# Performance work log

Measured on AMD Instinct MI355X. Metric: run time of the kernel, lower is better.

## Reference

```python
import jax, jax.numpy as jnp
import numpy as np

N_NODES = 100000
N_EDGES = 1600000
D_IN = 128
HID = 128
N_CLS = 10
N_GRAPHS = 128


def _gcn_conv(x, W, b, src, dst, dis, n):
    # x' = W x; out[i] = sum_{(j->i)} d_j^{-1/2} d_i^{-1/2} x'_j ; then + bias
    h = x @ W  # [N, out]
    norm = dis[src] * dis[dst]  # [E_tot]
    msg = h[src] * norm[:, None]  # gather + scale (irregular access)
    out = jax.ops.segment_sum(msg, dst, num_segments=n)  # scatter-add
    return out + b


def setup_inputs() -> dict:
    key = jax.random.key(0)
    ks = jax.random.split(key, 12)
    x = jax.random.normal(ks[0], (N_NODES, D_IN), dtype=jnp.float32)
    edge_index = jax.random.randint(ks[1], (2, N_EDGES), 0, N_NODES, dtype=jnp.int64)
    batch = jnp.sort(jax.random.randint(ks[2], (N_NODES,), 0, N_GRAPHS, dtype=jnp.int64))
    drop_u = jax.random.uniform(ks[3], (N_NODES, D_IN), dtype=jnp.float32)
    s = lambda k, sh, fan: jax.random.normal(k, sh, dtype=jnp.float32) / np.sqrt(fan)
    return {
        "x": x, "edge_index": edge_index, "batch": batch, "num_graphs": N_GRAPHS,
        "drop_u": drop_u,
        "lin1_w": s(ks[4], (D_IN, D_IN), D_IN), "lin1_b": jnp.zeros((D_IN,), jnp.float32),
        "conv1_w": s(ks[5], (D_IN, HID), D_IN), "conv1_b": jnp.zeros((HID,), jnp.float32),
        "conv2_w": s(ks[6], (HID, HID // 2), HID), "conv2_b": jnp.zeros((HID // 2,), jnp.float32),
        "lin2_w": s(ks[7], (HID // 2, N_CLS), HID // 2), "lin2_b": jnp.zeros((N_CLS,), jnp.float32),
    }


def reference(x, edge_index, batch, num_graphs, drop_u,
              lin1_w, lin1_b, conv1_w, conv1_b, conv2_w, conv2_b, lin2_w, lin2_b):
    n = x.shape[0]
    # add self loops (PyG GCNConv default)
    loop = jnp.arange(n, dtype=edge_index.dtype)
    src = jnp.concatenate([edge_index[0], loop])
    dst = jnp.concatenate([edge_index[1], loop])
    deg = jax.ops.segment_sum(jnp.ones_like(dst, dtype=x.dtype), dst, num_segments=n)
    dis = jnp.where(deg > 0, jax.lax.rsqrt(deg), 0.0)  # deg^{-1/2}

    h = x @ lin1_w + lin1_b
    h = _gcn_conv(h, conv1_w, conv1_b, src, dst, dis, n)
    # dropout p=0.5 (training mode in original): keep where u >= 0.5, scale by 2
    h = h * (drop_u >= 0.5).astype(h.dtype) * 2.0
    h = jax.nn.relu(h)
    h = _gcn_conv(h, conv2_w, conv2_b, src, dst, dis, n)
    # global mean pool over graph ids
    sums = jax.ops.segment_sum(h, batch, num_segments=num_graphs)
    cnts = jax.ops.segment_sum(jnp.ones((n,), h.dtype), batch, num_segments=num_graphs)
    pooled = sums / jnp.maximum(cnts, 1.0)[:, None]
    return pooled @ lin2_w + lin2_b
```

## Files before the change

### kernel.cpp

```cpp
#include <hip/hip_runtime.h>
#include <hip/hip_bf16.h>

#define DIN   128
#define HID2  64
#define NCLS  10
#define NGRAPH 128
#define SCAN_CHUNK 1024
#define NBLK 256
#define NBKT_MAX 512
#define CAP 6144

typedef __attribute__((ext_vector_type(8))) short bf16x8;
typedef __attribute__((ext_vector_type(4))) float f32x4;

__device__ __forceinline__ void atomAddF(float* p, float v) {
    unsafeAtomicAdd(p, v);
}

__device__ __forceinline__ unsigned short f2bf(float f) {
    unsigned int u = __float_as_uint(f);
    u += 0x7fffu + ((u >> 16) & 1u);
    return (unsigned short)(u >> 16);
}

__global__ __launch_bounds__(128) void k_w12(const float* __restrict__ lw,
                                             const float* __restrict__ lb,
                                             const float* __restrict__ cw,
                                             float* __restrict__ W12,
                                             float* __restrict__ c1preb) {
    int i = blockIdx.x, j = threadIdx.x;
    const float* arow = (i < 128) ? (lw + i * 128) : lb;
    float acc = 0.f;
#pragma unroll 8
    for (int k = 0; k < 128; ++k) acc += arow[k] * cw[k * 128 + j];
    if (i < 128) W12[i * 128 + j] = acc;
    else         c1preb[j] = acc;
}

__global__ __launch_bounds__(256) void k_zero(float* p, int n) {
    int i = blockIdx.x * 256 + threadIdx.x;
    if (i < n) p[i] = 0.0f;
}

__global__ __launch_bounds__(256) void k_bhist(const int* __restrict__ dst,
                                               int* __restrict__ bh, int E, int nbkt) {
    __shared__ int lh[NBKT_MAX];
    for (int i = threadIdx.x; i < nbkt; i += 256) lh[i] = 0;
    __syncthreads();
    for (int e = blockIdx.x * 256 + threadIdx.x; e < E; e += NBLK * 256)
        atomicAdd(&lh[__builtin_nontemporal_load(dst + e) >> 8], 1);
    __syncthreads();
    for (int i = threadIdx.x; i < nbkt; i += 256) bh[i * NBLK + blockIdx.x] = lh[i];
}

__global__ __launch_bounds__(256) void k_scan_part(const int* __restrict__ cnt,
                                                   int* __restrict__ part, int n) {
    int base = blockIdx.x * SCAN_CHUNK + threadIdx.x * 4;
    int s = 0;
#pragma unroll
    for (int j = 0; j < 4; ++j) { int i = base + j; if (i < n) s += cnt[i]; }
#pragma unroll
    for (int o = 32; o > 0; o >>= 1) s += __shfl_down(s, o);
    __shared__ int wsum[4];
    if ((threadIdx.x & 63) == 0) wsum[threadIdx.x >> 6] = s;
    __syncthreads();
    if (threadIdx.x == 0) part[blockIdx.x] = wsum[0] + wsum[1] + wsum[2] + wsum[3];
}
__global__ __launch_bounds__(256) void k_scan_mid(int* __restrict__ part,
                                                  int* __restrict__ total_out,
                                                  int B, int n) {
    __shared__ int sh[256];
    int t = threadIdx.x;
    int v = (t < B) ? part[t] : 0;
    sh[t] = v;
    __syncthreads();
    for (int off = 1; off < 256; off <<= 1) {
        int u = (t >= off) ? sh[t - off] : 0;
        __syncthreads();
        sh[t] += u;
        __syncthreads();
    }
    if (t < B) part[t] = sh[t] - v;
    if (t == 255) total_out[n] = sh[255];
}
__global__ __launch_bounds__(256) void k_scan_fin2(const int* cnt,
                                                   const int* __restrict__ part,
                                                   int* out, int n) {
    __shared__ int sh[256];
    int t = threadIdx.x;
    int base = blockIdx.x * SCAN_CHUNK + t * 4;
    int c[4]; int s = 0;
#pragma unroll
    for (int j = 0; j < 4; ++j) { int i = base + j; c[j] = (i < n) ? cnt[i] : 0; s += c[j]; }
    sh[t] = s;
    __syncthreads();
    for (int off = 1; off < 256; off <<= 1) {
        int u = (t >= off) ? sh[t - off] : 0;
        __syncthreads();
        sh[t] += u;
        __syncthreads();
    }
    int excl = part[blockIdx.x] + sh[t] - s;
#pragma unroll
    for (int j = 0; j < 4; ++j) {
        int i = base + j;
        if (i < n) out[i] = excl;
        excl += c[j];
    }
}

__global__ __launch_bounds__(256) void k_partition(const int* __restrict__ src,
                                                   const int* __restrict__ dst,
                                                   const int* __restrict__ bh,
                                                   int2* __restrict__ pairs, int E, int nbkt) {
    __shared__ int cur[NBKT_MAX];
    for (int i = threadIdx.x; i < nbkt; i += 256) cur[i] = bh[i * NBLK + blockIdx.x];
    __syncthreads();
    for (int e = blockIdx.x * 256 + threadIdx.x; e < E; e += NBLK * 256) {
        int d = __builtin_nontemporal_load(dst + e);
        int s = __builtin_nontemporal_load(src + e);
        int pos = atomicAdd(&cur[d >> 8], 1);
        pairs[pos] = make_int2(d, s);
    }
}

__global__ __launch_bounds__(256) void k_csr_local(const int2* __restrict__ pairs,
                                                   const int* __restrict__ bh,
                                                   int* __restrict__ row_start,
                                                   float* __restrict__ dis,
                                                   int* __restrict__ col,
                                                   int N) {
    __shared__ int cntL[256], scanL[256], curL[256];
    __shared__ int srcbuf[CAP];
    const int tid = threadIdx.x;
    const int lo = blockIdx.x << 8;
    const int bstart = bh[blockIdx.x * NBLK];
    const int bend = bh[(blockIdx.x + 1) * NBLK];
    const int nE = bend - bstart;

    cntL[tid] = 0;
    __syncthreads();
    for (int e = bstart + tid; e < bend; e += 256)
        atomicAdd(&cntL[pairs[e].x & 255], 1);
    __syncthreads();
    const int deg = cntL[tid];
    scanL[tid] = deg;
    __syncthreads();
    for (int off = 1; off < 256; off <<= 1) {
        int u = (tid >= off) ? scanL[tid - off] : 0;
        __syncthreads();
        scanL[tid] += u;
        __syncthreads();
    }
    const int excl = scanL[tid] - deg;
    curL[tid] = excl;
    const int node = lo + tid;
    if (node < N) {
        row_start[node] = bstart + excl;
        dis[node] = rsqrtf((float)(deg + 1));
    } else if (node == N) {
        row_start[N] = bend;
    }
    __syncthreads();
    if (nE <= CAP) {
        for (int e = bstart + tid; e < bend; e += 256) {
            int2 p = pairs[e];
            int pos = atomicAdd(&curL[p.x & 255], 1);
            srcbuf[pos] = p.y;
        }
        __syncthreads();
        for (int i = tid; i < nE; i += 256)
            col[bstart + i] = srcbuf[i];
    } else {
        for (int e = bstart + tid; e < bend; e += 256) {
            int2 p = pairs[e];
            int pos = atomicAdd(&curL[p.x & 255], 1);
            col[bstart + pos] = p.y;
        }
    }
}

template <int NCOL, bool MASK>
__global__ __launch_bounds__(256) void k_gemm_mfma(const float* __restrict__ A,
                                                   const float* __restrict__ W,
                                                   const float* __restrict__ bias,
                                                   const float* __restrict__ du,
                                                   unsigned short* __restrict__ out, int M) {
    constexpr int KP = 136;
    __shared__ unsigned short As[64 * KP];
    __shared__ unsigned short Wt[NCOL * KP];

    const int tid = threadIdx.x;
    const int row0 = blockIdx.x * 64;

    for (int f = tid; f < 2048; f += 256) {
        int r = f >> 5, c4 = f & 31;
        int gr = row0 + r;
        float4 v = make_float4(0.f, 0.f, 0.f, 0.f);
        if (gr < M) {
            v = *(const float4*)(A + (size_t)gr * 128 + c4 * 4);
            if (MASK) {
                float4 u = *(const float4*)(du + (size_t)gr * 128 + c4 * 4);
                v.x = (u.x >= 0.5f) ? 2.f * fmaxf(v.x, 0.f) : 0.f;
                v.y = (u.y >= 0.5f) ? 2.f * fmaxf(v.y, 0.f) : 0.f;
                v.z = (u.z >= 0.5f) ? 2.f * fmaxf(v.z, 0.f) : 0.f;
                v.w = (u.w >= 0.5f) ? 2.f * fmaxf(v.w, 0.f) : 0.f;
            }
        }
        ushort4 b;
        b.x = f2bf(v.x); b.y = f2bf(v.y); b.z = f2bf(v.z); b.w = f2bf(v.w);
        *(ushort4*)(&As[r * KP + c4 * 4]) = b;
    }
    for (int f = tid; f < 32 * NCOL; f += 256) {
        int k = f / (NCOL / 4), n4 = f % (NCOL / 4);
        float4 v = *(const float4*)(W + (size_t)k * NCOL + n4 * 4);
        Wt[(n4 * 4 + 0) * KP + k] = f2bf(v.x);
        Wt[(n4 * 4 + 1) * KP + k] = f2bf(v.y);
        Wt[(n4 * 4 + 2) * KP + k] = f2bf(v.z);
        Wt[(n4 * 4 + 3) * KP + k] = f2bf(v.w);
    }
    __syncthreads();

    const int wave = tid >> 6, lane = tid & 63;
    const int quad = lane >> 4, l16 = lane & 15;
    constexpr int CT = (NCOL == 128) ? 2 : 1;
    const int col0 = wave * 16 * CT;

    f32x4 acc[4][CT];
#pragma unroll
    for (int rt = 0; rt < 4; ++rt)
#pragma unroll
        for (int ct = 0; ct < CT; ++ct) acc[rt][ct] = 0.f;

#pragma unroll
    for (int ks = 0; ks < 4; ++ks) {
        const int kbase = ks * 32 + quad * 8;
        bf16x8 bfr[CT];
#pragma unroll
        for (int ct = 0; ct < CT; ++ct)
            bfr[ct] = *(const bf16x8*)(&Wt[(col0 + ct * 16 + l16) * KP + kbase]);
#pragma unroll
        for (int rt = 0; rt < 4; ++rt) {
            bf16x8 afr = *(const bf16x8*)(&As[(rt * 16 + l16) * KP + kbase]);
#pragma unroll
            for (int ct = 0; ct < CT; ++ct)
                acc[rt][ct] = __builtin_amdgcn_mfma_f32_16x16x32_bf16(afr, bfr[ct], acc[rt][ct], 0, 0, 0);
        }
    }

#pragma unroll
    for (int rt = 0; rt < 4; ++rt)
#pragma unroll
        for (int ct = 0; ct < CT; ++ct) {
            const int c = col0 + ct * 16 + l16;
            const float bv = bias ? bias[c] : 0.f;
#pragma unroll
            for (int reg = 0; reg < 4; ++reg) {
                const int gr = row0 + rt * 16 + quad * 4 + reg;
                if (gr < M) out[(size_t)gr * NCOL + c] = f2bf(acc[rt][ct][reg] + bv);
            }
        }
}

__device__ __forceinline__ void bfacc(uint4 v, float d, float* acc) {
    acc[0] = fmaf(d, __uint_as_float(v.x << 16),        acc[0]);
    acc[1] = fmaf(d, __uint_as_float(v.x & 0xffff0000u), acc[1]);
    acc[2] = fmaf(d, __uint_as_float(v.y << 16),        acc[2]);
    acc[3] = fmaf(d, __uint_as_float(v.y & 0xffff0000u), acc[3]);
    acc[4] = fmaf(d, __uint_as_float(v.z << 16),        acc[4]);
    acc[5] = fmaf(d, __uint_as_float(v.z & 0xffff0000u), acc[5]);
    acc[6] = fmaf(d, __uint_as_float(v.w << 16),        acc[6]);
    acc[7] = fmaf(d, __uint_as_float(v.w & 0xffff0000u), acc[7]);
}

template <int NCOL>
__global__ __launch_bounds__(256) void k_gather(const unsigned short* __restrict__ h,
                                                const int* __restrict__ row_start,
                                                const int* __restrict__ col,
                                                const float* __restrict__ dis,
                                                const float* __restrict__ bias,
                                                float* __restrict__ out, int n) {
    constexpr int LPN = NCOL / 8;
    const int node = (blockIdx.x * 256 + threadIdx.x) / LPN;
    const int l = threadIdx.x % LPN;
    if (node >= n) return;
    const int coff = l * 8;

    const float dn = dis[node];
    float acc[8];
    {
        uint4 v = *(const uint4*)(h + (size_t)node * NCOL + coff);
#pragma unroll
        for (int q = 0; q < 8; ++q) acc[q] = 0.f;
        bfacc(v, dn, acc);
    }

    const int beg = row_start[node], end = row_start[node + 1];
    int j = beg;
    for (; j + 1 < end; j += 2) {
        const int s0 = col[j], s1 = col[j + 1];
        const float d0 = dis[s0], d1 = dis[s1];
        const uint4 v0 = *(const uint4*)(h + (size_t)s0 * NCOL + coff);
        const uint4 v1 = *(const uint4*)(h + (size_t)s1 * NCOL + coff);
        bfacc(v0, d0, acc);
        bfacc(v1, d1, acc);
    }
    if (j < end) {
        const int s0 = col[j];
        const float d0 = dis[s0];
        const uint4 v0 = *(const uint4*)(h + (size_t)s0 * NCOL + coff);
        bfacc(v0, d0, acc);
    }

    float4 r0, r1;
    const float4 b0 = *(const float4*)(bias + coff);
    const float4 b1 = *(const float4*)(bias + coff + 4);
    r0.x = fmaf(dn, acc[0], b0.x); r0.y = fmaf(dn, acc[1], b0.y);
    r0.z = fmaf(dn, acc[2], b0.z); r0.w = fmaf(dn, acc[3], b0.w);
    r1.x = fmaf(dn, acc[4], b1.x); r1.y = fmaf(dn, acc[5], b1.y);
    r1.z = fmaf(dn, acc[6], b1.z); r1.w = fmaf(dn, acc[7], b1.w);
    float* o = out + (size_t)node * NCOL + coff;
    *(float4*)(o) = r0;
    *(float4*)(o + 4) = r1;
}

__global__ __launch_bounds__(256) void k_pool(const float* __restrict__ h,
                                              const int* __restrict__ batch,
                                              float* __restrict__ sums,
                                              float* __restrict__ cnt,
                                              int n) {
    int gid = (blockIdx.x * 256 + threadIdx.x) / 64;
    int f = threadIdx.x % 64;
    int ngroups = gridDim.x * 4;
    int per = (n + ngroups - 1) / ngroups;
    int start = gid * per;
    int end = min(n, start + per);
    if (start >= end) return;
    int cg = batch[start];
    float acc = 0.f;
    int count = 0;
    for (int i = start; i < end; ++i) {
        int b = batch[i];
        if (b != cg) {
            atomAddF(&sums[cg * 64 + f], acc);
            if (f == 0) atomAddF(&cnt[cg], (float)count);
            acc = 0.f; count = 0; cg = b;
        }
        acc += h[(size_t)i * 64 + f];
        ++count;
    }
    atomAddF(&sums[cg * 64 + f], acc);
    if (f == 0) atomAddF(&cnt[cg], (float)count);
}

__global__ __launch_bounds__(64) void k_final(const float* __restrict__ sums,
                                              const float* __restrict__ cnt,
                                              const float* __restrict__ w,
                                              const float* __restrict__ b,
                                              float* __restrict__ out) {
    int g = blockIdx.x, f = threadIdx.x;
    float c = fmaxf(cnt[g], 1.0f);
    float p = sums[g * 64 + f] / c;
#pragma unroll
    for (int cls = 0; cls < NCLS; ++cls) {
        float v = p * w[f * 10 + cls];
#pragma unroll
        for (int o = 32; o > 0; o >>= 1) v += __shfl_down(v, o);
        if (f == 0) out[g * 10 + cls] = v + b[cls];
    }
}

extern "C" void kernel_launch(void* const* d_in, const int* in_sizes, int n_in,
                              void* d_out, int out_size, void* d_ws, size_t ws_size,
                              hipStream_t stream) {
    const float* x       = (const float*)d_in[0];
    const int*   ei      = (const int*)d_in[1];
    const int*   batch   = (const int*)d_in[2];
    const float* drop_u  = (const float*)d_in[4];
    const float* lin1_w  = (const float*)d_in[5];
    const float* lin1_b  = (const float*)d_in[6];
    const float* conv1_w = (const float*)d_in[7];
    const float* conv1_b = (const float*)d_in[8];
    const float* conv2_w = (const float*)d_in[9];
    const float* conv2_b = (const float*)d_in[10];
    const float* lin2_w  = (const float*)d_in[11];
    const float* lin2_b  = (const float*)d_in[12];
    float* out = (float*)d_out;

    const int N = in_sizes[0] / DIN;
    const int E = in_sizes[1] / 2;
    const int* src = ei;
    const int* dst = ei + E;

    const int nbkt = (N + 255) >> 8;
    const int M = nbkt * NBLK;

    float* ws    = (float*)d_ws;
    float* out1  = ws;
    unsigned short* h1b = (unsigned short*)(ws + (size_t)N * 128);
    float* dis   = ws + (size_t)N * 128 + (size_t)N * 64;
    float* W12   = dis + N;
    float* c1pb  = W12 + 16384;
    float* sums  = c1pb + 128;
    float* cntp  = sums + NGRAPH * 64;
    int*   row_start = (int*)(cntp + NGRAPH);
    int*   part  = row_start + N + 2;
    int*   bh    = part + 256;
    int*   col   = bh + NBKT_MAX * NBLK + 2;
    int2*  pairs = (int2*)(col + E);
    unsigned short* h2b = h1b;
    float* out2  = out1;

    k_w12<<<129, 128, 0, stream>>>(lin1_w, lin1_b, conv1_w, W12, c1pb);

    k_bhist<<<NBLK, 256, 0, stream>>>(dst, bh, E, nbkt);
    const int scanB = (M + SCAN_CHUNK - 1) / SCAN_CHUNK;
    k_scan_part<<<scanB, 256, 0, stream>>>(bh, part, M);
    k_scan_mid<<<1, 256, 0, stream>>>(part, bh, scanB, M);
    k_scan_fin2<<<scanB, 256, 0, stream>>>(bh, part, bh, M);
    k_partition<<<NBLK, 256, 0, stream>>>(src, dst, bh, pairs, E, nbkt);
    k_csr_local<<<nbkt, 256, 0, stream>>>(pairs, bh, row_start, dis, col, N);

    const int gemmGrid = (N + 63) / 64;
    k_gemm_mfma<128, false><<<gemmGrid, 256, 0, stream>>>(x, W12, c1pb, nullptr, h1b, N);

    k_gather<128><<<((size_t)N * 16 + 255) / 256, 256, 0, stream>>>(h1b, row_start, col, dis, conv1_b, out1, N);

    k_gemm_mfma<64, true><<<gemmGrid, 256, 0, stream>>>(out1, conv2_w, nullptr, drop_u, h2b, N);

    k_gather<64><<<((size_t)N * 8 + 255) / 256, 256, 0, stream>>>(h2b, row_start, col, dis, conv2_b, out2, N);

    k_zero<<<(NGRAPH * 64 + NGRAPH + 255) / 256, 256, 0, stream>>>(sums, NGRAPH * 64 + NGRAPH);
    k_pool<<<2048, 256, 0, stream>>>(out2, batch, sums, cntp, N);
    k_final<<<NGRAPH, 64, 0, stream>>>(sums, cntp, lin2_w, lin2_b, out);
}
```

Baseline: 410.8 us.

## Pack edge pairs, bf16 intermediates, fuse pooling into second gather, drop zero kernel

Several changes at once. Edge pairs are packed into one 32-bit word (src<<8 | dst&255), which halves partition traffic. The first aggregation now writes bf16 instead of fp32, and a new GEMM reads bf16 with dropout/relu applied on load. The second gather fuses the global mean pool with wave-level reductions and atomics. The zeroing kernel moves into the histogram kernel, and the gather loops unroll by 4. Together these aim to cut memory traffic and launches, at the cost of extra bf16 rounding of the intermediate and a src-index range limit of 24 bits.

```diff
diff --git a/kernel.cpp b/kernel.cpp
--- a/kernel.cpp
+++ b/kernel.cpp
@@ -37,14 +37,12 @@
     else         c1preb[j] = acc;
 }
 
-__global__ __launch_bounds__(256) void k_zero(float* p, int n) {
-    int i = blockIdx.x * 256 + threadIdx.x;
-    if (i < n) p[i] = 0.0f;
-}
-
 __global__ __launch_bounds__(256) void k_bhist(const int* __restrict__ dst,
-                                               int* __restrict__ bh, int E, int nbkt) {
+                                               int* __restrict__ bh, int E, int nbkt,
+                                               float* __restrict__ zbuf, int zn) {
     __shared__ int lh[NBKT_MAX];
+    if (blockIdx.x == 0)
+        for (int i = threadIdx.x; i < zn; i += 256) zbuf[i] = 0.f;
     for (int i = threadIdx.x; i < nbkt; i += 256) lh[i] = 0;
     __syncthreads();
     for (int e = blockIdx.x * 256 + threadIdx.x; e < E; e += NBLK * 256)
@@ -112,7 +110,7 @@
 __global__ __launch_bounds__(256) void k_partition(const int* __restrict__ src,
                                                    const int* __restrict__ dst,
                                                    const int* __restrict__ bh,
-                                                   int2* __restrict__ pairs, int E, int nbkt) {
+                                                   int* __restrict__ pairs, int E, int nbkt) {
     __shared__ int cur[NBKT_MAX];
     for (int i = threadIdx.x; i < nbkt; i += 256) cur[i] = bh[i * NBLK + blockIdx.x];
     __syncthreads();
@@ -120,11 +118,11 @@
         int d = __builtin_nontemporal_load(dst + e);
         int s = __builtin_nontemporal_load(src + e);
         int pos = atomicAdd(&cur[d >> 8], 1);
-        pairs[pos] = make_int2(d, s);
-    }
-}
-
-__global__ __launch_bounds__(256) void k_csr_local(const int2* __restrict__ pairs,
+        pairs[pos] = (s << 8) | (d & 255);
+    }
+}
+
+__global__ __launch_bounds__(256) void k_csr_local(const int* __restrict__ pairs,
                                                    const int* __restrict__ bh,
                                                    int* __restrict__ row_start,
                                                    float* __restrict__ dis,
@@ -141,7 +139,7 @@
     cntL[tid] = 0;
     __syncthreads();
     for (int e = bstart + tid; e < bend; e += 256)
-        atomicAdd(&cntL[pairs[e].x & 255], 1);
+        atomicAdd(&cntL[pairs[e] & 255], 1);
     __syncthreads();
     const int deg = cntL[tid];
     scanL[tid] = deg;
@@ -164,27 +162,26 @@
     __syncthreads();
     if (nE <= CAP) {
         for (int e = bstart + tid; e < bend; e += 256) {
-            int2 p = pairs[e];
-            int pos = atomicAdd(&curL[p.x & 255], 1);
-            srcbuf[pos] = p.y;
+            int p = pairs[e];
+            int pos = atomicAdd(&curL[p & 255], 1);
+            srcbuf[pos] = ((unsigned int)p) >> 8;
         }
         __syncthreads();
         for (int i = tid; i < nE; i += 256)
             col[bstart + i] = srcbuf[i];
     } else {
         for (int e = bstart + tid; e < bend; e += 256) {
-            int2 p = pairs[e];
-            int pos = atomicAdd(&curL[p.x & 255], 1);
-            col[bstart + pos] = p.y;
-        }
-    }
-}
-
-template <int NCOL, bool MASK>
+            int p = pairs[e];
+            int pos = atomicAdd(&curL[p & 255], 1);
+            col[bstart + pos] = ((unsigned int)p) >> 8;
+        }
+    }
+}
+
+template <int NCOL>
 __global__ __launch_bounds__(256) void k_gemm_mfma(const float* __restrict__ A,
                                                    const float* __restrict__ W,
                                                    const float* __restrict__ bias,
-                                                   const float* __restrict__ du,
                                                    unsigned short* __restrict__ out, int M) {
     constexpr int KP = 136;
     __shared__ unsigned short As[64 * KP];
@@ -197,16 +194,7 @@
         int r = f >> 5, c4 = f & 31;
         int gr = row0 + r;
         float4 v = make_float4(0.f, 0.f, 0.f, 0.f);
-        if (gr < M) {
-            v = *(const float4*)(A + (size_t)gr * 128 + c4 * 4);
-            if (MASK) {
-                float4 u = *(const float4*)(du + (size_t)gr * 128 + c4 * 4);
-                v.x = (u.x >= 0.5f) ? 2.f * fmaxf(v.x, 0.f) : 0.f;
-                v.y = (u.y >= 0.5f) ? 2.f * fmaxf(v.y, 0.f) : 0.f;
-                v.z = (u.z >= 0.5f) ? 2.f * fmaxf(v.z, 0.f) : 0.f;
-                v.w = (u.w >= 0.5f) ? 2.f * fmaxf(v.w, 0.f) : 0.f;
-            }
-        }
+        if (gr < M) v = *(const float4*)(A + (size_t)gr * 128 + c4 * 4);
         ushort4 b;
         b.x = f2bf(v.x); b.y = f2bf(v.y); b.z = f2bf(v.z); b.w = f2bf(v.w);
         *(ushort4*)(&As[r * KP + c4 * 4]) = b;
@@ -260,6 +248,80 @@
                 if (gr < M) out[(size_t)gr * NCOL + c] = f2bf(acc[rt][ct][reg] + bv);
             }
         }
+}
+
+__device__ __forceinline__ unsigned int maskbf2(unsigned int w, float ua, float ub) {
+    float a = __uint_as_float(w << 16);
+    float b = __uint_as_float(w & 0xffff0000u);
+    a = (ua >= 0.5f) ? 2.f * fmaxf(a, 0.f) : 0.f;
+    b = (ub >= 0.5f) ? 2.f * fmaxf(b, 0.f) : 0.f;
+    return (unsigned int)f2bf(a) | ((unsigned int)f2bf(b) << 16);
+}
+
+__global__ __launch_bounds__(256) void k_gemm_bf16in(const unsigned short* __restrict__ A,
+                                                     const float* __restrict__ W,
+                                                     const float* __restrict__ du,
+                                                     unsigned short* __restrict__ out, int M) {
+    constexpr int NCOL = 64, KP = 136;
+    __shared__ unsigned short As[64 * KP];
+    __shared__ unsigned short Wt[NCOL * KP];
+
+    const int tid = threadIdx.x;
+    const int row0 = blockIdx.x * 64;
+
+    for (int f = tid; f < 1024; f += 256) {
+        int r = f >> 4, c8 = f & 15;
+        int gr = row0 + r;
+        uint4 b = make_uint4(0u, 0u, 0u, 0u);
+        if (gr < M) {
+            const uint4 v = *(const uint4*)(A + (size_t)gr * 128 + c8 * 8);
+            const float4 u0 = *(const float4*)(du + (size_t)gr * 128 + c8 * 8);
+            const float4 u1 = *(const float4*)(du + (size_t)gr * 128 + c8 * 8 + 4);
+            b.x = maskbf2(v.x, u0.x, u0.y);
+            b.y = maskbf2(v.y, u0.z, u0.w);
+            b.z = maskbf2(v.z, u1.x, u1.y);
+            b.w = maskbf2(v.w, u1.z, u1.w);
+        }
+        *(uint4*)(&As[r * KP + c8 * 8]) = b;
+    }
+    for (int f = tid; f < 32 * NCOL; f += 256) {
+        int k = f / (NCOL / 4), n4 = f % (NCOL / 4);
+        float4 v = *(const float4*)(W + (size_t)k * NCOL + n4 * 4);
+        Wt[(n4 * 4 + 0) * KP + k] = f2bf(v.x);
+        Wt[(n4 * 4 + 1) * KP + k] = f2bf(v.y);
+        Wt[(n4 * 4 + 2) * KP + k] = f2bf(v.z);
+        Wt[(n4 * 4 + 3) * KP + k] = f2bf(v.w);
+    }
+    __syncthreads();
+
+    const int wave = tid >> 6, lane = tid & 63;
+    const int quad = lane >> 4, l16 = lane & 15;
+    const int col0 = wave * 16;
+
+    f32x4 acc[4];
+#pragma unroll
+    for (int rt = 0; rt < 4; ++rt) acc[rt] = 0.f;
+
+#pragma unroll
+    for (int ks = 0; ks < 4; ++ks) {
+        const int kbase = ks * 32 + quad * 8;
+        bf16x8 bfr = *(const bf16x8*)(&Wt[(col0 + l16) * KP + kbase]);
+#pragma unroll
+        for (int rt = 0; rt < 4; ++rt) {
+            bf16x8 afr = *(const bf16x8*)(&As[(rt * 16 + l16) * KP + kbase]);
+            acc[rt] = __builtin_amdgcn_mfma_f32_16x16x32_bf16(afr, bfr, acc[rt], 0, 0, 0);
+        }
+    }
+
+#pragma unroll
+    for (int rt = 0; rt < 4; ++rt) {
+        const int c = col0 + l16;
+#pragma unroll
+        for (int reg = 0; reg < 4; ++reg) {
+            const int gr = row0 + rt * 16 + quad * 4 + reg;
+            if (gr < M) out[(size_t)gr * NCOL + c] = f2bf(acc[rt][reg]);
+        }
+    }
 }
 
 __device__ __forceinline__ void bfacc(uint4 v, float d, float* acc) {
@@ -273,23 +335,21 @@
     acc[7] = fmaf(d, __uint_as_float(v.w & 0xffff0000u), acc[7]);
 }
 
-template <int NCOL>
-__global__ __launch_bounds__(256) void k_gather(const unsigned short* __restrict__ h,
-                                                const int* __restrict__ row_start,
-                                                const int* __restrict__ col,
-                                                const float* __restrict__ dis,
-                                                const float* __restrict__ bias,
-                                                float* __restrict__ out, int n) {
-    constexpr int LPN = NCOL / 8;
-    const int node = (blockIdx.x * 256 + threadIdx.x) / LPN;
-    const int l = threadIdx.x % LPN;
+__global__ __launch_bounds__(256) void k_gather_h1(const unsigned short* __restrict__ h,
+                                                   const int* __restrict__ row_start,
+                                                   const int* __restrict__ col,
+                                                   const float* __restrict__ dis,
+                                                   const float* __restrict__ bias,
+                                                   unsigned short* __restrict__ outb, int n) {
+    const int node = (blockIdx.x * 256 + (int)threadIdx.x) >> 4;
+    const int l = threadIdx.x & 15;
     if (node >= n) return;
     const int coff = l * 8;
 
     const float dn = dis[node];
     float acc[8];
     {
-        uint4 v = *(const uint4*)(h + (size_t)node * NCOL + coff);
+        uint4 v = *(const uint4*)(h + (size_t)node * 128 + coff);
 #pragma unroll
         for (int q = 0; q < 8; ++q) acc[q] = 0.f;
         bfacc(v, dn, acc);
@@ -297,60 +357,115 @@
 
     const int beg = row_start[node], end = row_start[node + 1];
     int j = beg;
-    for (; j + 1 < end; j += 2) {
-        const int s0 = col[j], s1 = col[j + 1];
-        const float d0 = dis[s0], d1 = dis[s1];
-        const uint4 v0 = *(const uint4*)(h + (size_t)s0 * NCOL + coff);
-        const uint4 v1 = *(const uint4*)(h + (size_t)s1 * NCOL + coff);
+    for (; j + 3 < end; j += 4) {
+        const int s0 = col[j], s1 = col[j + 1], s2 = col[j + 2], s3 = col[j + 3];
+        const float d0 = dis[s0], d1 = dis[s1], d2 = dis[s2], d3 = dis[s3];
+        const uint4 v0 = *(const uint4*)(h + (size_t)s0 * 128 + coff);
+        const uint4 v1 = *(const uint4*)(h + (size_t)s1 * 128 + coff);
+        const uint4 v2 = *(const uint4*)(h + (size_t)s2 * 128 + coff);
+        const uint4 v3 = *(const uint4*)(h + (size_t)s3 * 128 + coff);
         bfacc(v0, d0, acc);
         bfacc(v1, d1, acc);
-    }
-    if (j < end) {
+        bfacc(v2, d2, acc);
+        bfacc(v3, d3, acc);
+    }
+    for (; j < end; ++j) {
         const int s0 = col[j];
         const float d0 = dis[s0];
-        const uint4 v0 = *(const uint4*)(h + (size_t)s0 * NCOL + coff);
+        const uint4 v0 = *(const uint4*)(h + (size_t)s0 * 128 + coff);
         bfacc(v0, d0, acc);
     }
 
-    float4 r0, r1;
     const float4 b0 = *(const float4*)(bias + coff);
     const float4 b1 = *(const float4*)(bias + coff + 4);
-    r0.x = fmaf(dn, acc[0], b0.x); r0.y = fmaf(dn, acc[1], b0.y);
-    r0.z = fmaf(dn, acc[2], b0.z); r0.w = fmaf(dn, acc[3], b0.w);
-    r1.x = fmaf(dn, acc[4], b1.x); r1.y = fmaf(dn, acc[5], b1.y);
-    r1.z = fmaf(dn, acc[6], b1.z); r1.w = fmaf(dn, acc[7], b1.w);
-    float* o = out + (size_t)node * NCOL + coff;
-    *(float4*)(o) = r0;
-    *(float4*)(o + 4) = r1;
-}
-
-__global__ __launch_bounds__(256) void k_pool(const float* __restrict__ h,
-                                              const int* __restrict__ batch,
-                                              float* __restrict__ sums,
-                                              float* __restrict__ cnt,
-                                              int n) {
-    int gid = (blockIdx.x * 256 + threadIdx.x) / 64;
-    int f = threadIdx.x % 64;
-    int ngroups = gridDim.x * 4;
-    int per = (n + ngroups - 1) / ngroups;
-    int start = gid * per;
-    int end = min(n, start + per);
-    if (start >= end) return;
-    int cg = batch[start];
-    float acc = 0.f;
-    int count = 0;
-    for (int i = start; i < end; ++i) {
-        int b = batch[i];
-        if (b != cg) {
-            atomAddF(&sums[cg * 64 + f], acc);
-            if (f == 0) atomAddF(&cnt[cg], (float)count);
-            acc = 0.f; count = 0; cg = b;
-        }
-        acc += h[(size_t)i * 64 + f];
-        ++count;
-    }
-    atomAddF(&sums[cg * 64 + f], acc);
-    if (f == 0) atomAddF(&cnt[cg], (float)count);
+    const float r0 = fmaf(dn, acc[0], b0.x), r1 = fmaf(dn, acc[1], b0.y);
+    const float r2 = fmaf(dn, acc[2], b0.z), r3 = fmaf(dn, acc[3], b0.w);
+    const float r4 = fmaf(dn, acc[4], b1.x), r5 = fmaf(dn, acc[5], b1.y);
+    const float r6 = fmaf(dn, acc[6], b1.z), r7 = fmaf(dn, acc[7], b1.w);
+    uint4 o;
+    o.x = (unsigned int)f2bf(r0) | ((unsigned int)f2bf(r1) << 16);
+    o.y = (unsigned int)f2bf(r2) | ((unsigned int)f2bf(r3) << 16);
+    o.z = (unsigned int)f2bf(r4) | ((unsigned int)f2bf(r5) << 16);
+    o.w = (unsigned int)f2bf(r6) | ((unsigned int)f2bf(r7) << 16);
+    *(uint4*)(outb + (size_t)node * 128 + coff) = o;
+}
+
+__global__ __launch_bounds__(256) void k_gather_pool(const unsigned short* __restrict__ h,
+                                                     const int* __restrict__ row_start,
+                                                     const int* __restrict__ col,
+                                                     const float* __restrict__ dis,
+                                                     const float* __restrict__ bias,
+                                                     const int* __restrict__ batch,
+                                                     float* __restrict__ sums,
+                                                     float* __restrict__ cnt, int n) {
+    const int node = (blockIdx.x * 256 + (int)threadIdx.x) >> 3;
+    const int l = threadIdx.x & 7;
+    const int coff = l * 8;
+    const bool valid = node < n;
+
+    float r[8];
+    int g = 0;
+    if (valid) {
+        const float dn = dis[node];
+        g = batch[node];
+        float acc[8];
+        {
+            uint4 v = *(const uint4*)(h + (size_t)node * 64 + coff);
+#pragma unroll
+            for (int q = 0; q < 8; ++q) acc[q] = 0.f;
+            bfacc(v, dn, acc);
+        }
+        const int beg = row_start[node], end = row_start[node + 1];
+        int j = beg;
+        for (; j + 3 < end; j += 4) {
+            const int s0 = col[j], s1 = col[j + 1], s2 = col[j + 2], s3 = col[j + 3];
+            const float d0 = dis[s0], d1 = dis[s1], d2 = dis[s2], d3 = dis[s3];
+            const uint4 v0 = *(const uint4*)(h + (size_t)s0 * 64 + coff);
+            const uint4 v1 = *(const uint4*)(h + (size_t)s1 * 64 + coff);
+            const uint4 v2 = *(const uint4*)(h + (size_t)s2 * 64 + coff);
+            const uint4 v3 = *(const uint4*)(h + (size_t)s3 * 64 + coff);
+            bfacc(v0, d0, acc);
+            bfacc(v1, d1, acc);
+            bfacc(v2, d2, acc);
+            bfacc(v3, d3, acc);
+        }
+        for (; j < end; ++j) {
+            const int s0 = col[j];
+            const float d0 = dis[s0];
+            const uint4 v0 = *(const uint4*)(h + (size_t)s0 * 64 + coff);
+            bfacc(v0, d0, acc);
+        }
+        const float4 b0 = *(const float4*)(bias + coff);
+        const float4 b1 = *(const float4*)(bias + coff + 4);
+        r[0] = fmaf(dn, acc[0], b0.x); r[1] = fmaf(dn, acc[1], b0.y);
+        r[2] = fmaf(dn, acc[2], b0.z); r[3] = fmaf(dn, acc[3], b0.w);
+        r[4] = fmaf(dn, acc[4], b1.x); r[5] = fmaf(dn, acc[5], b1.y);
+        r[6] = fmaf(dn, acc[6], b1.z); r[7] = fmaf(dn, acc[7], b1.w);
+    } else {
+#pragma unroll
+        for (int q = 0; q < 8; ++q) r[q] = 0.f;
+    }
+
+    const int g0 = __shfl(g, 0);
+    const bool uni = __all(valid && (g == g0));
+    if (uni) {
+#pragma unroll
+        for (int q = 0; q < 8; ++q) {
+            r[q] += __shfl_xor(r[q], 8);
+            r[q] += __shfl_xor(r[q], 16);
+            r[q] += __shfl_xor(r[q], 32);
+        }
+        const int lane = threadIdx.x & 63;
+        if (lane < 8) {
+#pragma unroll
+            for (int q = 0; q < 8; ++q) atomAddF(&sums[g0 * 64 + lane * 8 + q], r[q]);
+            if (lane == 0) atomAddF(&cnt[g0], 8.0f);
+        }
+    } else if (valid) {
+#pragma unroll
+        for (int q = 0; q < 8; ++q) atomAddF(&sums[g * 64 + coff + q], r[q]);
+        if (l == 0) atomAddF(&cnt[g], 1.0f);
+    }
 }
 
 __global__ __launch_bounds__(64) void k_final(const float* __restrict__ sums,
@@ -407,13 +522,13 @@
     int*   part  = row_start + N + 2;
     int*   bh    = part + 256;
     int*   col   = bh + NBKT_MAX * NBLK + 2;
-    int2*  pairs = (int2*)(col + E);
+    int*   pairs = col + E;
+    unsigned short* h1agg = (unsigned short*)out1;
     unsigned short* h2b = h1b;
-    float* out2  = out1;
 
     k_w12<<<129, 128, 0, stream>>>(lin1_w, lin1_b, conv1_w, W12, c1pb);
 
-    k_bhist<<<NBLK, 256, 0, stream>>>(dst, bh, E, nbkt);
+    k_bhist<<<NBLK, 256, 0, stream>>>(dst, bh, E, nbkt, sums, NGRAPH * 64 + NGRAPH);
     const int scanB = (M + SCAN_CHUNK - 1) / SCAN_CHUNK;
     k_scan_part<<<scanB, 256, 0, stream>>>(bh, part, M);
     k_scan_mid<<<1, 256, 0, stream>>>(part, bh, scanB, M);
@@ -422,15 +537,13 @@
     k_csr_local<<<nbkt, 256, 0, stream>>>(pairs, bh, row_start, dis, col, N);
 
     const int gemmGrid = (N + 63) / 64;
-    k_gemm_mfma<128, false><<<gemmGrid, 256, 0, stream>>>(x, W12, c1pb, nullptr, h1b, N);
-
-    k_gather<128><<<((size_t)N * 16 + 255) / 256, 256, 0, stream>>>(h1b, row_start, col, dis, conv1_b, out1, N);
-
-    k_gemm_mfma<64, true><<<gemmGrid, 256, 0, stream>>>(out1, conv2_w, nullptr, drop_u, h2b, N);
-
-    k_gather<64><<<((size_t)N * 8 + 255) / 256, 256, 0, stream>>>(h2b, row_start, col, dis, conv2_b, out2, N);
-
-    k_zero<<<(NGRAPH * 64 + NGRAPH + 255) / 256, 256, 0, stream>>>(sums, NGRAPH * 64 + NGRAPH);
-    k_pool<<<2048, 256, 0, stream>>>(out2, batch, sums, cntp, N);
+    k_gemm_mfma<128><<<gemmGrid, 256, 0, stream>>>(x, W12, c1pb, h1b, N);
+
+    k_gather_h1<<<((size_t)N * 16 + 255) / 256, 256, 0, stream>>>(h1b, row_start, col, dis, conv1_b, h1agg, N);
+
+    k_gemm_bf16in<<<gemmGrid, 256, 0, stream>>>(h1agg, conv2_w, drop_u, h2b, N);
+
+    k_gather_pool<<<((size_t)N * 8 + 255) / 256, 256, 0, stream>>>(h2b, row_start, col, dis, conv2_b, batch, sums, cntp, N);
+
     k_final<<<NGRAPH, 64, 0, stream>>>(sums, cntp, lin2_w, lin2_b, out);
 }
```

Measured after the change: 421.3 us. 2.6% more time.
